# Kernel tuning notes

Hardware: AMD Instinct MI355X
Metric: run time of the kernel (lower is better)

## Reference

```python
import jax, jax.numpy as jnp
import numpy as np

B, L, K = 4, 2048, 30
HID, EDGE, NL, NH = 128, 16, 3, 4
HD = HID // NH
SCALE = HD ** -0.5
LN_EPS = 1e-5


def setup_inputs() -> dict:
    key = jax.random.key(0)
    ks = jax.random.split(key, 16)
    s = 0.05
    d = {
        "h_nodes": jax.random.normal(ks[0], (B, L, HID), jnp.float32),
        "h_edges": jax.random.normal(ks[1], (B, L, K, EDGE), jnp.float32),
        "mask": jnp.ones((B, L), jnp.float32),
        "Wq": jax.random.normal(ks[2], (NL, HID, HID), jnp.float32) * s,
        "bq": jax.random.normal(ks[3], (NL, HID), jnp.float32) * s,
        "Wk": jax.random.normal(ks[4], (NL, HID, HID), jnp.float32) * s,
        "bk": jax.random.normal(ks[5], (NL, HID), jnp.float32) * s,
        "Wv": jax.random.normal(ks[6], (NL, HID, HID), jnp.float32) * s,
        "bv": jax.random.normal(ks[7], (NL, HID), jnp.float32) * s,
        "We": jax.random.normal(ks[8], (NL, EDGE, NH), jnp.float32) * s,
        "be": jax.random.normal(ks[9], (NL, NH), jnp.float32) * s,
        "Wo": jax.random.normal(ks[10], (NL, HID, HID), jnp.float32) * s,
        "bo": jax.random.normal(ks[11], (NL, HID), jnp.float32) * s,
        "ln_g": jnp.ones((NL, HID), jnp.float32),
        "ln_b": jnp.zeros((NL, HID), jnp.float32),
        "edge_idxs": jax.random.randint(ks[12], (B, L, K), 0, L, jnp.int32),
    }
    return d


def _layer_norm(x, g, b):
    mu = jnp.mean(x, axis=-1, keepdims=True)
    var = jnp.mean((x - mu) ** 2, axis=-1, keepdims=True)
    return (x - mu) * jax.lax.rsqrt(var + LN_EPS) * g + b


# per-batch gather of rows: a [L, ...], idx [L, K] -> [L, K, ...]
_gather = jax.vmap(lambda a, i: a[i])


def _forward(h_nodes, h_edges, mask, Wq, bq, Wk, bk, Wv, bv, We, be, Wo, bo, ln_g, ln_b, edge_idxs):
    neigh_mask = _gather(mask, edge_idxs)                     # [B,L,K]
    attn_mask = mask[:, None, :, None] * neigh_mask[:, None]  # [B,1,L,K]
    h = h_nodes
    for i in range(NL):
        hn = _gather(h, edge_idxs)                            # [B,L,K,HID]
        q = (h @ Wq[i] + bq[i]).reshape(B, L, NH, HD)
        k = (hn @ Wk[i] + bk[i]).reshape(B, L, K, NH, HD)
        v = (hn @ Wv[i] + bv[i]).reshape(B, L, K, NH, HD)
        scores = jnp.einsum('blhd,blkhd->bhlk', q, k) * SCALE
        scores = scores + jnp.transpose(h_edges @ We[i] + be[i], (0, 3, 1, 2))  # edge bias [B,NH,L,K]
        scores = jnp.where(attn_mask == 0, -1e9, scores)
        w = jax.nn.softmax(scores, axis=-1)                   # [B,NH,L,K]
        o = jnp.einsum('bhlk,blkhd->blhd', w, v).reshape(B, L, HID)
        o = o @ Wo[i] + bo[i]
        h = _layer_norm(h + o, ln_g[i], ln_b[i]) * mask[..., None]
    return h


def reference(h_nodes, h_edges, edge_idxs, mask, Wq, bq, Wk, bk, Wv, bv, We, be, Wo, bo, ln_g, ln_b):
    return _forward(h_nodes, h_edges, mask, Wq, bq, Wk, bk, Wv, bv, We, be, Wo, bo, ln_g, ln_b, edge_idxs)
```

## Files before the change

kernel.cpp:

```cpp
#include <hip/hip_runtime.h>
#include <math.h>

#define BB 4
#define LL 2048
#define KK 30
#define HIDD 128
#define EDGEE 16
#define NLL 3
#define NHH 4
#define SCALE_ 0.17677669529663687f
#define NROW 8192
#define NEDG 245760

typedef __attribute__((ext_vector_type(8))) short bf16x8;
typedef __attribute__((ext_vector_type(4))) float f32x4;

__device__ __forceinline__ ushort f2b(float f) {
    union { float f; uint u; } x; x.f = f;
    uint r = x.u + 0x7fff + ((x.u >> 16) & 1);
    return (ushort)(r >> 16);
}

__global__ __launch_bounds__(256) void prep_kernel(
    const float* __restrict__ Wq, const float* __restrict__ Wk,
    const float* __restrict__ Wv, const float* __restrict__ Wo,
    const float* __restrict__ h_edges, const float* __restrict__ We,
    const float* __restrict__ be, const float* __restrict__ h_nodes,
    ushort* __restrict__ WbT, float* __restrict__ eb, ushort* __restrict__ hb)
{
    const int id = blockIdx.x * 256 + threadIdx.x;
    if (blockIdx.y == 0) {
        if (id < 12 * 128 * 128) {
            int m = id >> 14;
            int rem = id & 16383;
            int k = rem >> 7, n = rem & 127;
            int layer = m >> 2, p = m & 3;
            const float* src;
            if (p == 0)      src = Wq + (size_t)layer * 16384;
            else if (p == 1) src = Wk + (size_t)layer * 16384;
            else if (p == 2) src = Wv + (size_t)layer * 16384;
            else             src = Wo + (size_t)layer * 16384;
            WbT[(size_t)m * 16384 + n * 128 + k] = f2b(src[k * 128 + n]);
        }
    } else if (blockIdx.y == 1) {
        __shared__ float We_s[NLL * EDGEE * NHH];
        __shared__ float be_s[NLL * NHH];
        if (threadIdx.x < NLL * EDGEE * NHH) We_s[threadIdx.x] = We[threadIdx.x];
        if (threadIdx.x < NLL * NHH) be_s[threadIdx.x] = be[threadIdx.x];
        __syncthreads();
        if (id < NEDG) {
            const float4* e4 = (const float4*)h_edges + (size_t)id * 4;
            float4 ec[4] = {e4[0], e4[1], e4[2], e4[3]};
            float ev[16];
            #pragma unroll
            for (int q = 0; q < 4; ++q) {
                ev[q * 4 + 0] = ec[q].x; ev[q * 4 + 1] = ec[q].y;
                ev[q * 4 + 2] = ec[q].z; ev[q * 4 + 3] = ec[q].w;
            }
            #pragma unroll
            for (int i = 0; i < NLL; ++i) {
                float r[NHH] = {be_s[i * 4], be_s[i * 4 + 1], be_s[i * 4 + 2], be_s[i * 4 + 3]};
                #pragma unroll
                for (int e = 0; e < EDGEE; ++e) {
                    float v = ev[e];
                    #pragma unroll
                    for (int hq = 0; hq < NHH; ++hq)
                        r[hq] = fmaf(v, We_s[i * 64 + e * NHH + hq], r[hq]);
                }
                ((float4*)eb)[(size_t)i * NEDG + id] = make_float4(r[0], r[1], r[2], r[3]);
            }
        }
    } else {
        float4 v = ((const float4*)h_nodes)[id];
        ushort4 o;
        o.x = f2b(v.x); o.y = f2b(v.y); o.z = f2b(v.z); o.w = f2b(v.w);
        ((ushort4*)hb)[id] = o;
    }
}

__global__ __launch_bounds__(256) void qkv_mfma(
    const ushort* __restrict__ hb, const ushort* __restrict__ WbT,
    const float* __restrict__ bq, const float* __restrict__ bk,
    const float* __restrict__ bv,
    float* __restrict__ Qp, float* __restrict__ Kp, float* __restrict__ Vp)
{
    __shared__ ushort As[128 * 128];
    __shared__ ushort Bs[128 * 128];

    const int t = threadIdx.x;
    const int proj = blockIdx.y;
    const ushort* W = WbT + (size_t)proj * 16384;
    const float* bias = proj == 0 ? bq : (proj == 1 ? bk : bv);
    float* out = proj == 0 ? Qp : (proj == 1 ? Kp : Vp);
    const int row0 = blockIdx.x * 128;

    const uint4* hb4 = (const uint4*)(hb + (size_t)row0 * 128);
    const uint4* W4 = (const uint4*)W;
    #pragma unroll
    for (int i = 0; i < 8; ++i) {
        int c = t + i * 256;
        int r = c >> 4, kc = c & 15;
        int off = (r * 256 + kc * 16) ^ ((r & 7) << 4);
        *(uint4*)((char*)As + off) = hb4[c];
        *(uint4*)((char*)Bs + off) = W4[c];
    }
    __syncthreads();

    const int wid = t >> 6, l = t & 63;
    const int lr = l & 15, lg = l >> 4;
    const int rbase = wid * 32;
    f32x4 acc[2][8];
    #pragma unroll
    for (int m = 0; m < 2; ++m)
        #pragma unroll
        for (int n = 0; n < 8; ++n) acc[m][n] = (f32x4){0.f, 0.f, 0.f, 0.f};

    #pragma unroll
    for (int ks = 0; ks < 4; ++ks) {
        const int kb = (lg * 8 + ks * 32) * 2;
        bf16x8 a[2], b[8];
        #pragma unroll
        for (int m = 0; m < 2; ++m) {
            int row = rbase + m * 16 + lr;
            a[m] = *(const bf16x8*)((const char*)As + ((row * 256 + kb) ^ ((row & 7) << 4)));
        }
        #pragma unroll
        for (int n = 0; n < 8; ++n) {
            int col = n * 16 + lr;
            b[n] = *(const bf16x8*)((const char*)Bs + ((col * 256 + kb) ^ ((col & 7) << 4)));
        }
        #pragma unroll
        for (int m = 0; m < 2; ++m)
            #pragma unroll
            for (int n = 0; n < 8; ++n)
                acc[m][n] = __builtin_amdgcn_mfma_f32_16x16x32_bf16(a[m], b[n], acc[m][n], 0, 0, 0);
    }

    #pragma unroll
    for (int n = 0; n < 8; ++n) {
        int col = n * 16 + lr;
        float bc = bias[col];
        #pragma unroll
        for (int m = 0; m < 2; ++m)
            #pragma unroll
            for (int r = 0; r < 4; ++r) {
                int row = row0 + rbase + m * 16 + lg * 4 + r;
                out[(size_t)row * 128 + col] = acc[m][n][r] + bc;
            }
    }
}

__global__ __launch_bounds__(256) void attn_kernel(
    const float* __restrict__ Qp, const float* __restrict__ Kp,
    const float* __restrict__ Vp,
    const int* __restrict__ edge_idxs, const float4* __restrict__ ebL,
    const float* __restrict__ mask, ushort* __restrict__ o_out)
{
    __shared__ int   widx[8][KK];
    __shared__ float ams[8][KK];
    __shared__ float ebs[8][KK][NHH];

    const int lbid = (blockIdx.x & 7) * 128 + (blockIdx.x >> 3);

    const int t = threadIdx.x;
    const int grp = t >> 5;
    const int g = t & 31;
    const int row = lbid * 8 + grp;
    const int b = row >> 11;
    const int hh = g >> 3;

    if (g < KK) {
        int gid = b * LL + edge_idxs[(size_t)row * KK + g];
        widx[grp][g] = gid;
        ams[grp][g] = mask[row] * mask[gid];
        *(float4*)&ebs[grp][g][0] = ebL[(size_t)row * KK + g];
    }
    __syncthreads();

    const float4* Kp4 = (const float4*)Kp;
    const float4* Vp4 = (const float4*)Vp;
    const float4 q4 = ((const float4*)Qp)[(size_t)row * 32 + g];

    float sc[KK];
    #pragma unroll
    for (int kb = 0; kb < 3; ++kb) {
        float4 kv[10];
        #pragma unroll
        for (int j = 0; j < 10; ++j)
            kv[j] = Kp4[(size_t)widx[grp][kb * 10 + j] * 32 + g];
        #pragma unroll
        for (int j = 0; j < 10; ++j) {
            int k = kb * 10 + j;
            float p = q4.x * kv[j].x + q4.y * kv[j].y + q4.z * kv[j].z + q4.w * kv[j].w;
            p += __shfl_xor(p, 4, 32);
            p += __shfl_xor(p, 2, 32);
            p += __shfl_xor(p, 1, 32);
            float am = ams[grp][k];
            float ebv = ebs[grp][k][hh];
            sc[k] = (am == 0.f) ? -1e9f : fmaf(p, SCALE_, ebv);
        }
    }

    float m = sc[0];
    #pragma unroll
    for (int k = 1; k < KK; ++k) m = fmaxf(m, sc[k]);
    float sum = 0.f;
    #pragma unroll
    for (int k = 0; k < KK; ++k) { sc[k] = __expf(sc[k] - m); sum += sc[k]; }
    const float inv = 1.f / sum;

    float4 o = make_float4(0.f, 0.f, 0.f, 0.f);
    #pragma unroll
    for (int kb = 0; kb < 3; ++kb) {
        float4 vv[10];
        #pragma unroll
        for (int j = 0; j < 10; ++j)
            vv[j] = Vp4[(size_t)widx[grp][kb * 10 + j] * 32 + g];
        #pragma unroll
        for (int j = 0; j < 10; ++j) {
            float w = sc[kb * 10 + j];
            o.x = fmaf(w, vv[j].x, o.x);
            o.y = fmaf(w, vv[j].y, o.y);
            o.z = fmaf(w, vv[j].z, o.z);
            o.w = fmaf(w, vv[j].w, o.w);
        }
    }
    ushort ob[4] = {f2b(o.x * inv), f2b(o.y * inv), f2b(o.z * inv), f2b(o.w * inv)};
    *(uint2*)&o_out[(size_t)row * HIDD + g * 4] = *(uint2*)ob;
}

__global__ __launch_bounds__(256) void outproj_mfma(
    const ushort* __restrict__ obb, const ushort* __restrict__ WoT,
    const float* __restrict__ bo, const float* __restrict__ hres,
    const float* __restrict__ g, const float* __restrict__ bb,
    const float* __restrict__ mask, float* __restrict__ hout,
    ushort* __restrict__ hbout)
{
    __shared__ ushort As[128 * 128];
    __shared__ ushort Bs[128 * 128];

    const int t = threadIdx.x;
    const int row0 = blockIdx.x * 128;

    const uint4* A4 = (const uint4*)(obb + (size_t)row0 * 128);
    const uint4* W4 = (const uint4*)WoT;
    #pragma unroll
    for (int i = 0; i < 8; ++i) {
        int c = t + i * 256;
        int r = c >> 4, kc = c & 15;
        int off = (r * 256 + kc * 16) ^ ((r & 7) << 4);
        *(uint4*)((char*)As + off) = A4[c];
        *(uint4*)((char*)Bs + off) = W4[c];
    }
    __syncthreads();

    const int wid = t >> 6, l = t & 63;
    const int lr = l & 15, lg = l >> 4;
    const int rbase = wid * 32;
    f32x4 acc[2][8];
    #pragma unroll
    for (int m = 0; m < 2; ++m)
        #pragma unroll
        for (int n = 0; n < 8; ++n) acc[m][n] = (f32x4){0.f, 0.f, 0.f, 0.f};

    #pragma unroll
    for (int ks = 0; ks < 4; ++ks) {
        const int kb = (lg * 8 + ks * 32) * 2;
        bf16x8 a[2], b[8];
        #pragma unroll
        for (int m = 0; m < 2; ++m) {
            int row = rbase + m * 16 + lr;
            a[m] = *(const bf16x8*)((const char*)As + ((row * 256 + kb) ^ ((row & 7) << 4)));
        }
        #pragma unroll
        for (int n = 0; n < 8; ++n) {
            int col = n * 16 + lr;
            b[n] = *(const bf16x8*)((const char*)Bs + ((col * 256 + kb) ^ ((col & 7) << 4)));
        }
        #pragma unroll
        for (int m = 0; m < 2; ++m)
            #pragma unroll
            for (int n = 0; n < 8; ++n)
                acc[m][n] = __builtin_amdgcn_mfma_f32_16x16x32_bf16(a[m], b[n], acc[m][n], 0, 0, 0);
    }

    float s1[2][4] = {}, s2[2][4] = {};
    #pragma unroll
    for (int n = 0; n < 8; ++n) {
        int col = n * 16 + lr;
        float boc = bo[col];
        #pragma unroll
        for (int m = 0; m < 2; ++m)
            #pragma unroll
            for (int r = 0; r < 4; ++r) {
                int row = row0 + rbase + m * 16 + lg * 4 + r;
                float v = acc[m][n][r] + boc + hres[(size_t)row * 128 + col];
                acc[m][n][r] = v;
                s1[m][r] += v;
                s2[m][r] += v * v;
            }
    }
    #pragma unroll
    for (int m = 0; m < 2; ++m)
        #pragma unroll
        for (int r = 0; r < 4; ++r) {
            float a = s1[m][r], b2 = s2[m][r];
            #pragma unroll
            for (int d = 1; d < 16; d <<= 1) {
                a  += __shfl_xor(a, d, 64);
                b2 += __shfl_xor(b2, d, 64);
            }
            s1[m][r] = a; s2[m][r] = b2;
        }

    float gv[8], bbv[8];
    #pragma unroll
    for (int n = 0; n < 8; ++n) { gv[n] = g[n * 16 + lr]; bbv[n] = bb[n * 16 + lr]; }

    #pragma unroll
    for (int m = 0; m < 2; ++m)
        #pragma unroll
        for (int r = 0; r < 4; ++r) {
            int row = row0 + rbase + m * 16 + lg * 4 + r;
            float mu = s1[m][r] * (1.f / 128.f);
            float var = s2[m][r] * (1.f / 128.f) - mu * mu;
            float rs = rsqrtf(var + 1e-5f);
            float mk = mask[row];
            #pragma unroll
            for (int n = 0; n < 8; ++n) {
                int col = n * 16 + lr;
                float val = ((acc[m][n][r] - mu) * rs * gv[n] + bbv[n]) * mk;
                hout[(size_t)row * 128 + col] = val;
                hbout[(size_t)row * 128 + col] = f2b(val);
            }
        }
}

extern "C" void kernel_launch(void* const* d_in, const int* in_sizes, int n_in,
                              void* d_out, int out_size, void* d_ws, size_t ws_size,
                              hipStream_t stream) {
    const float* h_nodes = (const float*)d_in[0];
    const float* h_edges = (const float*)d_in[1];
    const float* mask    = (const float*)d_in[2];
    const float* Wq = (const float*)d_in[3];
    const float* bq = (const float*)d_in[4];
    const float* Wk = (const float*)d_in[5];
    const float* bk = (const float*)d_in[6];
    const float* Wv = (const float*)d_in[7];
    const float* bv = (const float*)d_in[8];
    const float* We = (const float*)d_in[9];
    const float* be = (const float*)d_in[10];
    const float* Wo = (const float*)d_in[11];
    const float* bo = (const float*)d_in[12];
    const float* ln_g = (const float*)d_in[13];
    const float* ln_b = (const float*)d_in[14];
    const int* edge_idxs = (const int*)d_in[15];

    float* ws = (float*)d_ws;
    const size_t NE = (size_t)NROW * HIDD;
    float* h   = ws;
    float* Qp  = ws + NE;
    float* Kp  = ws + 2 * NE;
    float* Vp  = ws + 3 * NE;
    ushort* obb = (ushort*)(ws + 4 * NE);
    ushort* hb  = obb + NE;
    ushort* WbT = hb + NE;
    float* eb   = (float*)(WbT + 12 * 16384);

    prep_kernel<<<dim3(1024, 3), 256, 0, stream>>>(
        Wq, Wk, Wv, Wo, h_edges, We, be, h_nodes, WbT, eb, hb);

    for (int i = 0; i < NLL; ++i) {
        qkv_mfma<<<dim3(NROW / 128, 3), 256, 0, stream>>>(
            hb, WbT + (size_t)i * 4 * 16384,
            bq + i * HIDD, bk + i * HIDD, bv + i * HIDD,
            Qp, Kp, Vp);
        attn_kernel<<<NROW / 8, 256, 0, stream>>>(
            Qp, Kp, Vp, edge_idxs,
            (const float4*)eb + (size_t)i * NEDG, mask, obb);
        bool last = (i == NLL - 1);
        outproj_mfma<<<NROW / 128, 256, 0, stream>>>(
            obb, WbT + ((size_t)i * 4 + 3) * 16384, bo + i * HIDD,
            (i == 0) ? h_nodes : h,
            ln_g + i * HIDD, ln_b + i * HIDD, mask,
            last ? (float*)d_out : h, hb);
    }
}
```

Baseline: 96.66 us.

## Fuse K/V gathers with online softmax in neighbor attention kernel

Rewrites the per-node attention loop to load K and V rows together for each block of 10 neighbors and apply an online (streaming) softmax with running max and rescaling. It removes the separate second pass of V gathers and the 30-entry score array. More loads are in flight at once, which may hide gather latency better, at the cost of higher register pressure and extra exp/rescale work per block.

Measured after the change: 110.3 us. +14.1%, slower.

```diff
diff --git a/kernel.cpp b/kernel.cpp
--- a/kernel.cpp
+++ b/kernel.cpp
@@ -181,13 +181,19 @@
     const float4* Vp4 = (const float4*)Vp;
     const float4 q4 = ((const float4*)Qp)[(size_t)row * 32 + g];
 
-    float sc[KK];
+    float m = -1e30f, sum = 0.f;
+    float4 o = make_float4(0.f, 0.f, 0.f, 0.f);
+
     #pragma unroll
     for (int kb = 0; kb < 3; ++kb) {
-        float4 kv[10];
-        #pragma unroll
-        for (int j = 0; j < 10; ++j)
-            kv[j] = Kp4[(size_t)widx[grp][kb * 10 + j] * 32 + g];
+        float4 kv[10], vv[10];
+        #pragma unroll
+        for (int j = 0; j < 10; ++j) {
+            size_t base = (size_t)widx[grp][kb * 10 + j] * 32 + g;
+            kv[j] = Kp4[base];
+            vv[j] = Vp4[base];
+        }
+        float s[10];
         #pragma unroll
         for (int j = 0; j < 10; ++j) {
             int k = kb * 10 + j;
@@ -197,34 +203,27 @@
             p += __shfl_xor(p, 1, 32);
             float am = ams[grp][k];
             float ebv = ebs[grp][k][hh];
-            sc[k] = (am == 0.f) ? -1e9f : fmaf(p, SCALE_, ebv);
-        }
-    }
-
-    float m = sc[0];
-    #pragma unroll
-    for (int k = 1; k < KK; ++k) m = fmaxf(m, sc[k]);
-    float sum = 0.f;
-    #pragma unroll
-    for (int k = 0; k < KK; ++k) { sc[k] = __expf(sc[k] - m); sum += sc[k]; }
-    const float inv = 1.f / sum;
-
-    float4 o = make_float4(0.f, 0.f, 0.f, 0.f);
-    #pragma unroll
-    for (int kb = 0; kb < 3; ++kb) {
-        float4 vv[10];
-        #pragma unroll
-        for (int j = 0; j < 10; ++j)
-            vv[j] = Vp4[(size_t)widx[grp][kb * 10 + j] * 32 + g];
+            s[j] = (am == 0.f) ? -1e9f : fmaf(p, SCALE_, ebv);
+        }
+        float bm = s[0];
+        #pragma unroll
+        for (int j = 1; j < 10; ++j) bm = fmaxf(bm, s[j]);
+        float mn = fmaxf(m, bm);
+        float f = __expf(m - mn);
+        sum *= f;
+        o.x *= f; o.y *= f; o.z *= f; o.w *= f;
+        m = mn;
         #pragma unroll
         for (int j = 0; j < 10; ++j) {
-            float w = sc[kb * 10 + j];
+            float w = __expf(s[j] - mn);
+            sum += w;
             o.x = fmaf(w, vv[j].x, o.x);
             o.y = fmaf(w, vv[j].y, o.y);
             o.z = fmaf(w, vv[j].z, o.z);
             o.w = fmaf(w, vv[j].w, o.w);
         }
     }
+    const float inv = 1.f / sum;
     ushort ob[4] = {f2b(o.x * inv), f2b(o.y * inv), f2b(o.z * inv), f2b(o.w * inv)};
     *(uint2*)&o_out[(size_t)row * HIDD + g * 4] = *(uint2*)ob;
 }
```
